# Kernel tuning notes

Measured on AMD Instinct MI355X. Metric: run time of the kernel, lower is better.

## Reference

```python
import jax, jax.numpy as jnp
import numpy as np

DIM = 1536
HEADS = 8
DK = 64            # key_size
DV = DIM // HEADS  # value_size = 192
NPF = 32           # num_rel_pos_features
LN_EPS = 1e-3


def central_mask_features(positions, features, seq_len):
    # Borzoi/baskerville central-mask positional basis
    pow_rate = jnp.exp(jnp.log(seq_len + 1.0) / features)
    center_widths = pow_rate ** jnp.arange(1, features + 1, dtype=jnp.float32)
    return (center_widths[None, :] > jnp.abs(positions)[:, None]).astype(jnp.float32)


def get_positional_embed(n, feature_size):
    distances = jnp.arange(-n + 1, n, dtype=jnp.float32)  # (2n-1,)
    emb = central_mask_features(distances, feature_size // 2, n)
    return jnp.concatenate([emb, jnp.sign(distances)[:, None] * emb], axis=-1)  # (2n-1, F)


def relative_shift(x):
    # x: (b, h, n, 2n-1) -> (b, h, n, n), Transformer-XL shift trick
    b, h, t1, t2 = x.shape
    x = jnp.pad(x, ((0, 0), (0, 0), (0, 0), (1, 0)))  # (b,h,n,2n)
    x = x.reshape(b, h, t2 + 1, t1)[:, :, 1:, :]       # (b,h,2n-1,n)
    x = x.reshape(b, h, t1, t2)
    return x[..., :((t2 + 1) // 2)]


def setup_inputs() -> dict:
    key = jax.random.key(0)
    ks = jax.random.split(key, 10)
    s = 0.02
    return {
        "x": jax.random.normal(ks[0], (1, 4096, DIM), jnp.float32),
        "ln_gamma": jnp.ones((DIM,), jnp.float32),
        "ln_beta": jnp.zeros((DIM,), jnp.float32),
        "Wq": jax.random.normal(ks[1], (DIM, HEADS * DK), jnp.float32) * s,
        "Wk": jax.random.normal(ks[2], (DIM, HEADS * DK), jnp.float32) * s,
        "Wv": jax.random.normal(ks[3], (DIM, HEADS * DV), jnp.float32) * s,
        "Wr": jax.random.normal(ks[4], (NPF, HEADS * DK), jnp.float32) * s,
        "Wo": jax.random.normal(ks[5], (HEADS * DV, DIM), jnp.float32) * s,
        "bo": jnp.zeros((DIM,), jnp.float32),
        "rel_content_bias": jax.random.normal(ks[6], (1, HEADS, 1, DK), jnp.float32),
        "rel_pos_bias": jax.random.normal(ks[7], (1, HEADS, 1, DK), jnp.float32),
    }


def reference(x, ln_gamma, ln_beta, Wq, Wk, Wv, Wr, Wo, bo, rel_content_bias, rel_pos_bias):
    B, N, D = x.shape
    # LayerNorm(eps=1e-3)
    mu = jnp.mean(x, axis=-1, keepdims=True)
    var = jnp.mean(jnp.square(x - mu), axis=-1, keepdims=True)
    xn = (x - mu) * jax.lax.rsqrt(var + LN_EPS) * ln_gamma + ln_beta
    # projections -> (B,H,N,d)
    q = (xn @ Wq).reshape(B, N, HEADS, DK).transpose(0, 2, 1, 3) * (DK ** -0.5)
    k = (xn @ Wk).reshape(B, N, HEADS, DK).transpose(0, 2, 1, 3)
    v = (xn @ Wv).reshape(B, N, HEADS, DV).transpose(0, 2, 1, 3)
    content_logits = jnp.einsum('bhid,bhjd->bhij', q + rel_content_bias, k)
    # relative positions (dropout is identity in eval mode)
    pos = get_positional_embed(N, NPF)                       # (2N-1, NPF)
    rel_k = (pos @ Wr).reshape(2 * N - 1, HEADS, DK).transpose(1, 0, 2)  # (H,2N-1,DK)
    rel_logits = jnp.einsum('bhid,hjd->bhij', q + rel_pos_bias, rel_k)   # (B,H,N,2N-1)
    rel_logits = relative_shift(rel_logits)                  # (B,H,N,N)
    attn = jax.nn.softmax(content_logits + rel_logits, axis=-1)
    out = jnp.einsum('bhij,bhjd->bhid', attn, v)
    out = out.transpose(0, 2, 1, 3).reshape(B, N, HEADS * DV)
    return out @ Wo + bo
```

## Files before the change

### kernel.cpp

```cpp
#include <hip/hip_runtime.h>
#include <hip/hip_bf16.h>
#include <math.h>

typedef __hip_bfloat16 bf16;
typedef __attribute__((ext_vector_type(8))) short bf16x8;
typedef __attribute__((ext_vector_type(4))) float f32x4;

#define DIMX 1536
#define NSEQ 4096
#define NHEAD 8
#define DKH 64
#define DVH 192
#define HDK 512
#define HDV 1536
#define KSPLIT 2
#define KVB 32

static __device__ __forceinline__ float b2f(bf16 x){ return __bfloat162float(x); }
static __device__ __forceinline__ bf16 f2b(float x){ return __float2bfloat16(x); }

#define GLD_TO_LDS(gsrc, ldst) __builtin_amdgcn_global_load_lds( \
    (const __attribute__((address_space(1))) unsigned int*)(gsrc), \
    (__attribute__((address_space(3))) unsigned int*)(ldst), 16, 0, 0)

static __device__ __forceinline__ int xcd_swz(int b, int nwg){
  return (b & 7)*(nwg>>3) + (b>>3);
}

__global__ __launch_bounds__(256) void k_cvtT(const float* __restrict__ W, bf16* __restrict__ WT, int K, int N){
  __shared__ float t[32][33];
  int n0 = blockIdx.x<<5, k0 = blockIdx.y<<5;
  int tx = threadIdx.x & 31, ty = threadIdx.x >> 5;
  #pragma unroll
  for (int r=ty; r<32; r+=8) t[r][tx] = W[(size_t)(k0+r)*N + n0 + tx];
  __syncthreads();
  #pragma unroll
  for (int r=ty; r<32; r+=8) WT[(size_t)(n0+r)*K + k0 + tx] = f2b(t[tx][r]);
}

__global__ __launch_bounds__(256) void k_T(const bf16* __restrict__ src, bf16* __restrict__ dst, int R, int C){
  __shared__ bf16 t[64][65];
  int c0 = blockIdx.x<<6, r0 = blockIdx.y<<6;
  int tx = threadIdx.x & 63, ty = threadIdx.x >> 6;
  for (int r=ty; r<64; r+=4) t[r][tx] = src[(size_t)(r0+r)*C + c0 + tx];
  __syncthreads();
  for (int r=ty; r<64; r+=4){
    int dv = c0+r, kv = r0+tx;
    int kvp = (kv & ~31) | ((((kv>>3)&3) ^ ((dv>>1)&3))<<3) | (kv&7);
    dst[(size_t)dv*R + kvp] = t[tx][r];
  }
}

__global__ __launch_bounds__(256) void k_ln(const float* __restrict__ x, const float* __restrict__ g,
                                            const float* __restrict__ b,
                                            bf16* __restrict__ xnh, bf16* __restrict__ xnl){
  int row = blockIdx.x, t = threadIdx.x;
  const float* xr = x + (size_t)row*DIMX;
  float v[6]; float s=0.f, ss=0.f;
  #pragma unroll
  for (int j=0;j<6;++j){ v[j]=xr[t+256*j]; s+=v[j]; ss+=v[j]*v[j]; }
  int lane = t&63, wave = t>>6;
  #pragma unroll
  for (int off=32; off>0; off>>=1){ s += __shfl_down(s,off,64); ss += __shfl_down(ss,off,64); }
  __shared__ float red[8];
  if (lane==0){ red[wave]=s; red[wave+4]=ss; }
  __syncthreads();
  s = red[0]+red[1]+red[2]+red[3];
  ss = red[4]+red[5]+red[6]+red[7];
  float mu = s*(1.f/DIMX);
  float var = ss*(1.f/DIMX) - mu*mu;
  float rstd = rsqrtf(var + 1e-3f);
  #pragma unroll
  for (int j=0;j<6;++j){
    int c = t+256*j;
    float xv = (v[j]-mu)*rstd*g[c] + b[c];
    bf16 hi = f2b(xv);
    xnh[(size_t)row*DIMX + c] = hi;
    xnl[(size_t)row*DIMX + c] = f2b(xv - b2f(hi));
  }
}

template<int EPI>
__global__ __launch_bounds__(256) void k_gemm(const bf16* __restrict__ A, const bf16* __restrict__ BT,
    void* __restrict__ Cout, const float* __restrict__ bias, int M, int N, int K)
{
  __shared__ bf16 As[128][32];
  __shared__ bf16 Bs[128][32];
  int nbx = N>>7;
  int bid = xcd_swz(blockIdx.x, gridDim.x);
  int m0 = (bid / nbx)<<7, n0 = (bid % nbx)<<7;
  int tid = threadIdx.x, wave = tid>>6, lane = tid&63;
  int lr = lane&15, lc = lane>>4;
  int wm = (wave>>1)<<6, wn = (wave&1)<<6;
  f32x4 acc[4][4] = {};
  for (int k0=0; k0<K; k0+=32){
    __syncthreads();
    #pragma unroll
    for (int it=0; it<2; ++it){
      int id = tid + (it<<8);
      int rr = id>>2, cc = id&3;
      unsigned wbase = (unsigned)(((it<<8) + (tid & 192))*16);
      GLD_TO_LDS(A  + (size_t)(m0+rr)*K + k0 + cc*8, (char*)As + wbase);
      GLD_TO_LDS(BT + (size_t)(n0+rr)*K + k0 + cc*8, (char*)Bs + wbase);
    }
    __syncthreads();
    bf16x8 af[4], bfr[4];
    #pragma unroll
    for (int mt=0; mt<4; ++mt) af[mt] = *(const bf16x8*)(&As[wm + mt*16 + lr][lc*8]);
    #pragma unroll
    for (int nt=0; nt<4; ++nt) bfr[nt] = *(const bf16x8*)(&Bs[wn + nt*16 + lr][lc*8]);
    #pragma unroll
    for (int mt=0; mt<4; ++mt)
      #pragma unroll
      for (int nt=0; nt<4; ++nt)
        acc[mt][nt] = __builtin_amdgcn_mfma_f32_16x16x32_bf16(af[mt], bfr[nt], acc[mt][nt], 0,0,0);
  }
  #pragma unroll
  for (int mt=0; mt<4; ++mt){
    #pragma unroll
    for (int nt=0; nt<4; ++nt){
      #pragma unroll
      for (int reg=0; reg<4; ++reg){
        int row = m0 + wm + mt*16 + (lc<<2) + reg;
        int col = n0 + wn + nt*16 + lr;
        if (EPI==0) ((bf16*)Cout)[(size_t)row*N + col] = f2b(acc[mt][nt][reg]);
        else        ((float*)Cout)[(size_t)row*N + col] = acc[mt][nt][reg] + bias[col];
      }
    }
  }
}

__global__ __launch_bounds__(256) void k_gemmqk(const bf16* __restrict__ Ahi, const bf16* __restrict__ Alo,
    const bf16* __restrict__ Bhi,
    bf16* __restrict__ qph, bf16* __restrict__ qpl,
    bf16* __restrict__ kh, bf16* __restrict__ kl, const float* __restrict__ cb)
{
  __shared__ bf16 Ash[128][32];
  __shared__ bf16 Asl[128][32];
  __shared__ bf16 Bsh[128][32];
  const int N = 1024, K = DIMX, nbx = 8;
  int bid = xcd_swz(blockIdx.x, gridDim.x);
  int m0 = (bid / nbx)<<7, n0 = (bid % nbx)<<7;
  int tid = threadIdx.x, wave = tid>>6, lane = tid&63;
  int lr = lane&15, lc = lane>>4;
  int wm = (wave>>1)<<6, wn = (wave&1)<<6;
  f32x4 acc[4][4] = {};
  for (int k0=0; k0<K; k0+=32){
    __syncthreads();
    #pragma unroll
    for (int it=0; it<2; ++it){
      int id = tid + (it<<8);
      int rr = id>>2, cc = id&3;
      unsigned wbase = (unsigned)(((it<<8) + (tid & 192))*16);
      size_t ga = (size_t)(m0+rr)*K + k0 + cc*8;
      size_t gb = (size_t)(n0+rr)*K + k0 + cc*8;
      GLD_TO_LDS(Ahi + ga, (char*)Ash + wbase);
      GLD_TO_LDS(Alo + ga, (char*)Asl + wbase);
      GLD_TO_LDS(Bhi + gb, (char*)Bsh + wbase);
    }
    __syncthreads();
    bf16x8 ah[4], al[4], bh[4];
    #pragma unroll
    for (int mt=0; mt<4; ++mt){
      ah[mt] = *(const bf16x8*)(&Ash[wm + mt*16 + lr][lc*8]);
      al[mt] = *(const bf16x8*)(&Asl[wm + mt*16 + lr][lc*8]);
    }
    #pragma unroll
    for (int nt=0; nt<4; ++nt)
      bh[nt] = *(const bf16x8*)(&Bsh[wn + nt*16 + lr][lc*8]);
    #pragma unroll
    for (int mt=0; mt<4; ++mt)
      #pragma unroll
      for (int nt=0; nt<4; ++nt){
        acc[mt][nt] = __builtin_amdgcn_mfma_f32_16x16x32_bf16(ah[mt], bh[nt], acc[mt][nt], 0,0,0);
        acc[mt][nt] = __builtin_amdgcn_mfma_f32_16x16x32_bf16(al[mt], bh[nt], acc[mt][nt], 0,0,0);
      }
  }
  bool isQ = (n0 < 512);
  #pragma unroll
  for (int mt=0; mt<4; ++mt){
    #pragma unroll
    for (int nt=0; nt<4; ++nt){
      #pragma unroll
      for (int reg=0; reg<4; ++reg){
        int row = m0 + wm + mt*16 + (lc<<2) + reg;
        int col = n0 + wn + nt*16 + lr;
        float v = acc[mt][nt][reg];
        if (isQ){
          v = v*0.125f + cb[col];
          bf16 hi = f2b(v);
          qph[(size_t)row*HDK + col] = hi;
          qpl[(size_t)row*HDK + col] = f2b(v - b2f(hi));
        } else {
          int ck = col - 512;
          int colw = (ck & ~63) | ((((ck>>3)&7) ^ (row&7))<<3) | (ck&7);
          bf16 hi = f2b(v);
          kh[(size_t)row*HDK + colw] = hi;
          kl[(size_t)row*HDK + colw] = f2b(v - b2f(hi));
        }
      }
    }
  }
}

__global__ __launch_bounds__(256) void k_abtab(const bf16* __restrict__ qph, const bf16* __restrict__ qpl,
                                               const float* __restrict__ Wr,
                                               const float* __restrict__ cb, const float* __restrict__ pb,
                                               float* __restrict__ ab){
  int i = blockIdx.x, t = threadIdx.x;
  __shared__ float qpp[HDK];
  __shared__ float us[NHEAD][32];
  #pragma unroll
  for (int j=0;j<2;++j){
    int c = t + j*256;
    size_t qi = (size_t)i*HDK + c;
    qpp[c] = b2f(qph[qi]) + b2f(qpl[qi]) - cb[c] + pb[c];
  }
  __syncthreads();
  {
    int h = t>>5, f = t&31;
    const float* wr = Wr + (size_t)f*HDK + h*DKH;
    const float* qh = qpp + h*DKH;
    float u = 0.f;
    #pragma unroll
    for (int d=0; d<64; d+=4){
      float4 w4 = *(const float4*)(wr + d);
      u += w4.x*qh[d] + w4.y*qh[d+1] + w4.z*qh[d+2] + w4.w*qh[d+3];
    }
    us[h][f] = u;
  }
  __syncthreads();
  if (t < 128){
    int h2 = t>>4, f2 = t&15;
    float a=0.f, bb=0.f;
    for (int g=15; g>=f2; --g){ a += us[h2][g]; bb += us[h2][16+g]; }
    float* o = ab + ((size_t)h2*NSEQ + i)*34;
    o[f2] = a + bb;
    o[17+f2] = a - bb;
    if (f2 == 0){ o[16] = a; o[33] = a; }
  }
}

__global__ __launch_bounds__(256,4) void k_attn(
    const bf16* __restrict__ qph, const bf16* __restrict__ qpl,
    const bf16* __restrict__ khs, const bf16* __restrict__ kls,
    const bf16* __restrict__ vts, const float* __restrict__ ab,
    bf16* __restrict__ PO, float2* __restrict__ ML)
{
  int wg = blockIdx.x;
  int h  = wg & 7;
  int qtile = (wg >> 3) & 63;
  int ks = wg >> 9;
  int q0 = qtile * 64;
  int tid = threadIdx.x, wave = tid>>6, lane = tid&63;
  int lr = lane&15, lc = lane>>4;

  __shared__ bf16 Ksh[KVB][64];
  __shared__ bf16 Ksl[KVB][64];
  __shared__ bf16 Vs[DVH][KVB];
  __shared__ bf16 Ps[4][16][36];
  __shared__ float Ts[64][34];

  {
    const float* src = ab + ((size_t)h*NSEQ + q0)*34;
    for (int xx=tid; xx<64*34; xx+=256) ((float*)Ts)[xx] = src[xx];
  }

  bf16x8 qfh[2], qfl[2];
  {
    int row = q0 + wave*16 + lr;
    const bf16* qrh = qph + (size_t)row*HDK + h*DKH;
    const bf16* qrl = qpl + (size_t)row*HDK + h*DKH;
    qfh[0] = *(const bf16x8*)(qrh + 8*lc);
    qfh[1] = *(const bf16x8*)(qrh + 32 + 8*lc);
    qfl[0] = *(const bf16x8*)(qrl + 8*lc);
    qfl[1] = *(const bf16x8*)(qrl + 32 + 8*lc);
  }
  const bf16* Kh = khs + h*DKH;
  const bf16* Kl = kls + h*DKH;
  const bf16* Vt = vts + (size_t)h*DVH*NSEQ;

  f32x4 oacc[12] = {};
  float mrow[4], lrow[4];
  #pragma unroll
  for (int r=0;r<4;++r){ mrow[r]=-3e38f; lrow[r]=0.f; }

  const float RCPL = 1.33329424f;
  int kv_lo = ks * (NSEQ/KSPLIT);
  int kv_hi = kv_lo + NSEQ/KSPLIT;

  for (int kv0=kv_lo; kv0<kv_hi; kv0+=KVB) {
    __syncthreads();
    {
      int r = tid>>3, c = tid&7;
      size_t gk = (size_t)(kv0+r)*HDK + c*8;
      GLD_TO_LDS(Kh + gk, (char*)Ksh + (tid&192)*16);
      GLD_TO_LDS(Kl + gk, (char*)Ksl + (tid&192)*16);
      #pragma unroll
      for (int j=0; j<3; ++j){
        int id = j*256 + tid;
        int vr = id>>2, vc = id&3;
        GLD_TO_LDS(Vt + (size_t)vr*NSEQ + kv0 + vc*8, (char*)Vs + (j*256 + (tid&192))*16);
      }
    }
    __syncthreads();

    f32x4 sf[2];
    #pragma unroll
    for (int ct=0; ct<2; ++ct){
      f32x4 s = {};
      int krow = ct*16 + lr;
      int sw0 = ((lc  ) ^ (krow&7))*8;
      int sw1 = ((lc+4) ^ (krow&7))*8;
      bf16x8 kh0 = *(const bf16x8*)(&Ksh[krow][sw0]);
      bf16x8 kh1 = *(const bf16x8*)(&Ksh[krow][sw1]);
      bf16x8 kl0 = *(const bf16x8*)(&Ksl[krow][sw0]);
      bf16x8 kl1 = *(const bf16x8*)(&Ksl[krow][sw1]);
      s = __builtin_amdgcn_mfma_f32_16x16x32_bf16(qfh[0], kh0, s, 0,0,0);
      s = __builtin_amdgcn_mfma_f32_16x16x32_bf16(qfh[1], kh1, s, 0,0,0);
      s = __builtin_amdgcn_mfma_f32_16x16x32_bf16(qfl[0], kh0, s, 0,0,0);
      s = __builtin_amdgcn_mfma_f32_16x16x32_bf16(qfl[1], kh1, s, 0,0,0);
      s = __builtin_amdgcn_mfma_f32_16x16x32_bf16(qfh[0], kl0, s, 0,0,0);
      s = __builtin_amdgcn_mfma_f32_16x16x32_bf16(qfh[1], kl1, s, 0,0,0);
      sf[ct]=s;
    }
    int tmin = kv0 - q0 - 63, tmax = kv0 - q0 + 31;
    int slotu = -1;
    if (tmin >= 1){
      int g1 = (int)(__log2f((float)tmin) * RCPL);
      int g2 = (int)(__log2f((float)tmax) * RCPL);
      if (g1 == g2) slotu = g1;
    } else if (tmax <= -1){
      int g1 = (int)(__log2f((float)(-tmax)) * RCPL);
      int g2 = (int)(__log2f((float)(-tmin)) * RCPL);
      if (g1 == g2) slotu = 17 + g1;
    }
    float mnew[4];
    #pragma unroll
    for (int r=0;r<4;++r) mnew[r]=mrow[r];
    if (slotu >= 0){
      float bu[4];
      #pragma unroll
      for (int reg=0; reg<4; ++reg) bu[reg] = Ts[wave*16 + 4*lc + reg][slotu];
      #pragma unroll
      for (int ct=0; ct<2; ++ct){
        #pragma unroll
        for (int reg=0; reg<4; ++reg){
          float sv = sf[ct][reg] + bu[reg];
          sf[ct][reg] = sv;
          mnew[reg] = fmaxf(mnew[reg], sv);
        }
      }
    } else {
      #pragma unroll
      for (int ct=0; ct<2; ++ct){
        int j = kv0 + ct*16 + lr;
        #pragma unroll
        for (int reg=0; reg<4; ++reg){
          int rowloc = wave*16 + 4*lc + reg;
          int dd = j - (q0 + rowloc);
          int ad = dd<0 ? -dd : dd;
          int gg = ad ? (int)(__log2f((float)ad) * RCPL) : 16;
          float bias = Ts[rowloc][(dd<0 ? 17:0) + gg];
          float sv = sf[ct][reg] + bias;
          sf[ct][reg] = sv;
          mnew[reg] = fmaxf(mnew[reg], sv);
        }
      }
    }
    #pragma unroll
    for (int off=1; off<16; off<<=1){
      #pragma unroll
      for (int r=0;r<4;++r) mnew[r] = fmaxf(mnew[r], __shfl_xor(mnew[r], off, 64));
    }
    bool okl = true;
    #pragma unroll
    for (int r=0;r<4;++r) okl = okl && (mnew[r] - mrow[r] <= 8.f);
    if (!__all(okl)){
      float scl[4];
      #pragma unroll
      for (int r=0;r<4;++r){
        scl[r] = __expf(mrow[r]-mnew[r]);
        mrow[r]=mnew[r];
        lrow[r]*=scl[r];
      }
      #pragma unroll
      for (int t12=0;t12<12;++t12){
        #pragma unroll
        for (int reg=0;reg<4;++reg) oacc[t12][reg]*=scl[reg];
      }
    }
    #pragma unroll
    for (int ct=0; ct<2; ++ct){
      #pragma unroll
      for (int reg=0; reg<4; ++reg){
        float p = __expf(sf[ct][reg]-mrow[reg]);
        lrow[reg]+=p;
        Ps[wave][4*lc+reg][ct*16+lr] = f2b(p);
      }
    }
    bf16x8 pa = *(const bf16x8*)(&Ps[wave][lr][lc*8]);
    #pragma unroll
    for (int t12=0; t12<12; ++t12){
      int vrow = t12*16 + lr;
      bf16x8 v0 = *(const bf16x8*)(&Vs[vrow][(lc ^ ((vrow>>1)&3))*8]);
      oacc[t12] = __builtin_amdgcn_mfma_f32_16x16x32_bf16(pa, v0, oacc[t12], 0,0,0);
    }
  }
  #pragma unroll
  for (int off=1; off<16; off<<=1){
    #pragma unroll
    for (int r=0;r<4;++r) lrow[r] += __shfl_xor(lrow[r], off, 64);
  }
  #pragma unroll
  for (int t12=0;t12<12;++t12){
    #pragma unroll
    for (int reg=0;reg<4;++reg){
      int rowloc = wave*16 + 4*lc + reg;
      PO[((size_t)wg*64 + rowloc)*DVH + t12*16 + lr] = f2b(oacc[t12][reg]);
    }
  }
  if (lr == 0){
    #pragma unroll
    for (int reg=0; reg<4; ++reg){
      int rowloc = wave*16 + 4*lc + reg;
      ML[(size_t)wg*64 + rowloc] = make_float2(mrow[reg], lrow[reg]);
    }
  }
}

__global__ __launch_bounds__(256) void k_comb(const bf16* __restrict__ PO, const float2* __restrict__ ML,
                                              bf16* __restrict__ Obuf){
  int i = blockIdx.x;
  int qtile = i>>6, rl = i&63;
  for (int c=threadIdx.x; c<HDV; c+=256){
    int h = c/DVH, d = c - h*DVH;
    int wg0 = qtile*8 + h, wg1 = 512 + wg0;
    float2 ml0 = ML[(size_t)wg0*64 + rl];
    float2 ml1 = ML[(size_t)wg1*64 + rl];
    float M = fmaxf(ml0.x, ml1.x);
    float w0 = __expf(ml0.x - M), w1 = __expf(ml1.x - M);
    float l = ml0.y*w0 + ml1.y*w1;
    float o = b2f(PO[((size_t)wg0*64 + rl)*DVH + d])*w0
            + b2f(PO[((size_t)wg1*64 + rl)*DVH + d])*w1;
    Obuf[(size_t)i*HDV + c] = f2b(o / l);
  }
}

extern "C" void kernel_launch(void* const* d_in, const int* in_sizes, int n_in,
                              void* d_out, int out_size, void* d_ws, size_t ws_size,
                              hipStream_t stream) {
  const float* x  = (const float*)d_in[0];
  const float* lg = (const float*)d_in[1];
  const float* lb = (const float*)d_in[2];
  const float* Wq = (const float*)d_in[3];
  const float* Wk = (const float*)d_in[4];
  const float* Wv = (const float*)d_in[5];
  const float* Wr = (const float*)d_in[6];
  const float* Wo = (const float*)d_in[7];
  const float* bo = (const float*)d_in[8];
  const float* cb = (const float*)d_in[9];
  const float* pb = (const float*)d_in[10];
  float* out = (float*)d_out;

  char* ws = (char*)d_ws;
  size_t off = 0;
  auto alloc = [&](size_t bytes)->void*{ void* p = ws + off; off += (bytes + 255) & ~(size_t)255; return p; };
  bf16* WoT  = (bf16*)alloc((size_t)DIMX*HDV*2);
  bf16* qph  = (bf16*)alloc((size_t)NSEQ*HDK*2);
  bf16* qpl  = (bf16*)alloc((size_t)NSEQ*HDK*2);
  bf16* kh   = (bf16*)alloc((size_t)NSEQ*HDK*2);
  bf16* kl   = (bf16*)alloc((size_t)NSEQ*HDK*2);
  bf16* vt   = (bf16*)alloc((size_t)HDV*NSEQ*2);
  float* ab  = (float*)alloc((size_t)NHEAD*NSEQ*34*4);
  bf16* Obuf = (bf16*)alloc((size_t)NSEQ*HDV*2);
  float2* ML = (float2*)alloc((size_t)KSPLIT*512*64*sizeof(float2));
  char* scratch = (char*)alloc(0);
  bf16* xnh  = (bf16*)alloc((size_t)NSEQ*DIMX*2);
  bf16* xnl  = (bf16*)alloc((size_t)NSEQ*DIMX*2);
  bf16* v_rm = (bf16*)alloc((size_t)NSEQ*HDV*2);
  bf16* WqkT = (bf16*)alloc((size_t)1024*DIMX*2);
  bf16* WvT  = (bf16*)alloc((size_t)HDV*DIMX*2);
  bf16* PO   = (bf16*)scratch;
  (void)in_sizes; (void)n_in; (void)out_size; (void)ws_size;

  k_cvtT<<<dim3(HDK/32,  DIMX/32), 256, 0, stream>>>(Wq, WqkT, DIMX, HDK);
  k_cvtT<<<dim3(HDK/32,  DIMX/32), 256, 0, stream>>>(Wk, WqkT + (size_t)512*DIMX, DIMX, HDK);
  k_cvtT<<<dim3(HDV/32,  DIMX/32), 256, 0, stream>>>(Wv, WvT, DIMX, HDV);
  k_cvtT<<<dim3(DIMX/32, HDV/32),  256, 0, stream>>>(Wo, WoT, HDV, DIMX);
  k_ln<<<NSEQ, 256, 0, stream>>>(x, lg, lb, xnh, xnl);

  k_gemmqk<<<(NSEQ/128)*(1024/128), 256, 0, stream>>>(xnh, xnl, WqkT, qph, qpl, kh, kl, cb);
  k_gemm<0><<<(NSEQ/128)*(HDV/128), 256, 0, stream>>>(xnh, WvT, (void*)v_rm, nullptr, NSEQ, HDV, DIMX);

  k_abtab<<<NSEQ, 256, 0, stream>>>(qph, qpl, Wr, cb, pb, ab);
  k_T<<<dim3(HDV/64, NSEQ/64), 256, 0, stream>>>(v_rm, vt, NSEQ, HDV);

  k_attn<<<KSPLIT*512, 256, 0, stream>>>(qph, qpl, kh, kl, vt, ab, PO, ML);
  k_comb<<<NSEQ, 256, 0, stream>>>(PO, ML, Obuf);

  k_gemm<1><<<(NSEQ/128)*(DIMX/128), 256, 0, stream>>>(Obuf, WoT, (void*)out, bo, NSEQ, DIMX, HDV);
}
```

Before: 497.0 us.

## Double-buffer K/V tiles in attention loop with async prefetch and MFMA priority

After: 534.3 us. 1.08x slower.

```diff
diff --git a/kernel.cpp b/kernel.cpp
--- a/kernel.cpp
+++ b/kernel.cpp
@@ -241,7 +241,7 @@
   }
 }
 
-__global__ __launch_bounds__(256,4) void k_attn(
+__global__ __launch_bounds__(256,3) void k_attn(
     const bf16* __restrict__ qph, const bf16* __restrict__ qpl,
     const bf16* __restrict__ khs, const bf16* __restrict__ kls,
     const bf16* __restrict__ vts, const float* __restrict__ ab,
@@ -255,9 +255,9 @@
   int tid = threadIdx.x, wave = tid>>6, lane = tid&63;
   int lr = lane&15, lc = lane>>4;
 
-  __shared__ bf16 Ksh[KVB][64];
-  __shared__ bf16 Ksl[KVB][64];
-  __shared__ bf16 Vs[DVH][KVB];
+  __shared__ bf16 Ksh[2][KVB][64];
+  __shared__ bf16 Ksl[2][KVB][64];
+  __shared__ bf16 Vs[2][DVH][KVB];
   __shared__ bf16 Ps[4][16][36];
   __shared__ float Ts[64][34];
 
@@ -289,33 +289,38 @@
   int kv_lo = ks * (NSEQ/KSPLIT);
   int kv_hi = kv_lo + NSEQ/KSPLIT;
 
+  auto STAGE = [&](int buf, int kv0){
+    int r = tid>>3, c = tid&7;
+    size_t gk = (size_t)(kv0+r)*HDK + c*8;
+    GLD_TO_LDS(Kh + gk, (char*)(&Ksh[buf][0][0]) + (tid&192)*16);
+    GLD_TO_LDS(Kl + gk, (char*)(&Ksl[buf][0][0]) + (tid&192)*16);
+    #pragma unroll
+    for (int j=0; j<3; ++j){
+      int id = j*256 + tid;
+      int vr = id>>2, vc = id&3;
+      GLD_TO_LDS(Vt + (size_t)vr*NSEQ + kv0 + vc*8, (char*)(&Vs[buf][0][0]) + (j*256 + (tid&192))*16);
+    }
+  };
+
+  STAGE(0, kv_lo);
+  __syncthreads();
+  int cur = 0;
+
   for (int kv0=kv_lo; kv0<kv_hi; kv0+=KVB) {
-    __syncthreads();
-    {
-      int r = tid>>3, c = tid&7;
-      size_t gk = (size_t)(kv0+r)*HDK + c*8;
-      GLD_TO_LDS(Kh + gk, (char*)Ksh + (tid&192)*16);
-      GLD_TO_LDS(Kl + gk, (char*)Ksl + (tid&192)*16);
-      #pragma unroll
-      for (int j=0; j<3; ++j){
-        int id = j*256 + tid;
-        int vr = id>>2, vc = id&3;
-        GLD_TO_LDS(Vt + (size_t)vr*NSEQ + kv0 + vc*8, (char*)Vs + (j*256 + (tid&192))*16);
-      }
-    }
-    __syncthreads();
+    if (kv0 + KVB < kv_hi) STAGE(cur^1, kv0 + KVB);
 
     f32x4 sf[2];
+    __builtin_amdgcn_s_setprio(1);
     #pragma unroll
     for (int ct=0; ct<2; ++ct){
       f32x4 s = {};
       int krow = ct*16 + lr;
       int sw0 = ((lc  ) ^ (krow&7))*8;
       int sw1 = ((lc+4) ^ (krow&7))*8;
-      bf16x8 kh0 = *(const bf16x8*)(&Ksh[krow][sw0]);
-      bf16x8 kh1 = *(const bf16x8*)(&Ksh[krow][sw1]);
-      bf16x8 kl0 = *(const bf16x8*)(&Ksl[krow][sw0]);
-      bf16x8 kl1 = *(const bf16x8*)(&Ksl[krow][sw1]);
+      bf16x8 kh0 = *(const bf16x8*)(&Ksh[cur][krow][sw0]);
+      bf16x8 kh1 = *(const bf16x8*)(&Ksh[cur][krow][sw1]);
+      bf16x8 kl0 = *(const bf16x8*)(&Ksl[cur][krow][sw0]);
+      bf16x8 kl1 = *(const bf16x8*)(&Ksl[cur][krow][sw1]);
       s = __builtin_amdgcn_mfma_f32_16x16x32_bf16(qfh[0], kh0, s, 0,0,0);
       s = __builtin_amdgcn_mfma_f32_16x16x32_bf16(qfh[1], kh1, s, 0,0,0);
       s = __builtin_amdgcn_mfma_f32_16x16x32_bf16(qfl[0], kh0, s, 0,0,0);
@@ -324,6 +329,7 @@
       s = __builtin_amdgcn_mfma_f32_16x16x32_bf16(qfh[1], kl1, s, 0,0,0);
       sf[ct]=s;
     }
+    __builtin_amdgcn_s_setprio(0);
     int tmin = kv0 - q0 - 63, tmax = kv0 - q0 + 31;
     int slotu = -1;
     if (tmin >= 1){
@@ -400,12 +406,17 @@
       }
     }
     bf16x8 pa = *(const bf16x8*)(&Ps[wave][lr][lc*8]);
+    __builtin_amdgcn_s_setprio(1);
     #pragma unroll
     for (int t12=0; t12<12; ++t12){
       int vrow = t12*16 + lr;
-      bf16x8 v0 = *(const bf16x8*)(&Vs[vrow][(lc ^ ((vrow>>1)&3))*8]);
+      bf16x8 v0 = *(const bf16x8*)(&Vs[cur][vrow][(lc ^ ((vrow>>1)&3))*8]);
       oacc[t12] = __builtin_amdgcn_mfma_f32_16x16x32_bf16(pa, v0, oacc[t12], 0,0,0);
     }
+    __builtin_amdgcn_s_setprio(0);
+
+    __syncthreads();
+    cur ^= 1;
   }
   #pragma unroll
   for (int off=1; off<16; off<<=1){
```
